# Kernel tuning notes

Hardware: AMD Instinct MI355X
Metric: run time of the kernel (lower is better)

The kernel has to match this reference:

```python
import jax, jax.numpy as jnp
import numpy as np

B, S, Dm, H, W, G = 2, 4096, 768, 12, 256, 16
HD = Dm // H
NEG = -10000.0


def _band_qk(q, k, w):
    # q,k: [B,S,H,D] -> banded scores [B,S,H,2w+1]; slot j = key position i-w+j
    Bq, Sq, Hq, Dq = q.shape
    nb = Sq // w
    qb = q.reshape(Bq, nb, w, Hq, Dq)
    kp = jnp.pad(k, ((0, 0), (w, w), (0, 0), (0, 0)))
    idx = (jnp.arange(nb) * w)[:, None] + jnp.arange(3 * w)[None, :]
    kb = kp[:, idx]                                    # [B,nb,3w,H,D]
    s = jnp.einsum('btxhd,btyhd->bthxy', qb, kb)       # [B,nb,H,w,3w]
    r = jnp.arange(w)[:, None]
    c = r + jnp.arange(2 * w + 1)[None, :]
    band = s[..., r, c]                                # [B,nb,H,w,2w+1]
    return band.transpose(0, 1, 3, 2, 4).reshape(Bq, Sq, Hq, 2 * w + 1)


def _band_pv(p, v, w):
    # p: [B,S,H,2w+1], v: [B,S,H,D] -> [B,S,H,D]
    Bp, Sp, Hp, _ = p.shape
    Dv = v.shape[-1]
    nb = Sp // w
    vp = jnp.pad(v, ((0, 0), (w, w), (0, 0), (0, 0)))
    idx = (jnp.arange(nb) * w)[:, None] + jnp.arange(3 * w)[None, :]
    vb = vp[:, idx]                                    # [B,nb,3w,H,D]
    pb = p.reshape(Bp, nb, w, Hp, 2 * w + 1).transpose(0, 1, 3, 2, 4)
    r = jnp.arange(w)[:, None]
    c = r + jnp.arange(2 * w + 1)[None, :]
    pband = jnp.zeros((Bp, nb, Hp, w, 3 * w), p.dtype).at[..., r, c].set(pb)
    out = jnp.einsum('bthxy,btyhd->btxhd', pband, vb)  # [B,nb,w,H,D]
    return out.reshape(Bp, Sp, Hp, Dv)


def setup_inputs() -> dict:
    key = jax.random.key(0)
    ks = jax.random.split(key, 13)
    inp = {'hidden_states': jax.random.normal(ks[0], (B, S, Dm), dtype=jnp.float32)}
    names = ['Wq', 'bq', 'Wk', 'bk', 'Wv', 'bv', 'Wqg', 'bqg', 'Wkg', 'bkg', 'Wvg', 'bvg']
    for i, n in enumerate(names):
        sh = (Dm, Dm) if n.startswith('W') else (Dm,)
        inp[n] = 0.02 * jax.random.normal(ks[i + 1], sh, dtype=jnp.float32)
    inp['n_global'] = G
    return inp


def reference(hidden_states, Wq, bq, Wk, bk, Wv, bv, Wqg, bqg, Wkg, bkg, Wvg, bvg, n_global):
    Bh, Sh, D = hidden_states.shape
    hd = D // H
    w, g = W, n_global
    scale = 1.0 / jnp.sqrt(jnp.float32(hd))
    q = ((hidden_states @ Wq + bq) * scale).reshape(Bh, Sh, H, hd)
    k = (hidden_states @ Wk + bk).reshape(Bh, Sh, H, hd)
    v = (hidden_states @ Wv + bv).reshape(Bh, Sh, H, hd)
    # banded local attention scores (mask_invalid_locations -> -inf outside seq)
    band = _band_qk(q, k, w)                           # [B,S,H,2w+1]
    i = jnp.arange(Sh)[:, None]
    j = jnp.arange(2 * w + 1)[None, :]
    kpos = i - w + j                                   # key position per window slot
    valid = (kpos >= 0) & (kpos < Sh)
    band = jnp.where(valid[None, :, None, :], band, -jnp.inf)
    # remove global keys from windowed attention (-10000 float mask)
    band = band + jnp.where(valid & (kpos < g), NEG, 0.0)[None, :, None, :]
    # global columns: every query attends to global keys (local k projection)
    sel = jnp.einsum('bihd,bghd->bihg', q, k[:, :g])
    logits = jnp.concatenate([sel, band], axis=-1)     # [B,S,H,g+2w+1]
    probs = jax.nn.softmax(logits.astype(jnp.float32), axis=-1)
    attn = jnp.einsum('bihg,bghd->bihd', probs[..., :g], v[:, :g])
    attn = attn + _band_pv(probs[..., g:], v, w)       # [B,S,H,hd]
    # global token rows: full attention with global projections
    qg = ((hidden_states[:, :g] @ Wqg + bqg) * scale).reshape(Bh, g, H, hd)
    kg = (hidden_states @ Wkg + bkg).reshape(Bh, Sh, H, hd)
    vg = (hidden_states @ Wvg + bvg).reshape(Bh, Sh, H, hd)
    gl = jnp.einsum('bghd,bshd->bhgs', qg, kg)
    gp = jax.nn.softmax(gl.astype(jnp.float32), axis=-1)
    out_g = jnp.einsum('bhgs,bshd->bghd', gp, vg)      # [B,g,H,hd]
    attn = attn.at[:, :g].set(out_g)
    return attn.reshape(Bh, Sh, D)
```

## Files before the change

### kernel.cpp

```cpp
#include <hip/hip_runtime.h>

constexpr int Bc = 2, Sc = 4096, Dmc = 768, Hc = 12, HDc = 64, Wc = 256, Gc = 16;
constexpr int NCH = 16, CHK = 256;
constexpr float LOG2E = 1.4426950408889634f;
constexpr float SCALEc = 0.125f;
constexpr float SCALE2q = 0.125f * LOG2E;
constexpr float NEG2c = -10000.0f * LOG2E;

typedef __attribute__((ext_vector_type(8))) short s16x8;
typedef __attribute__((ext_vector_type(4))) short s16x4;
typedef __attribute__((ext_vector_type(4))) float f32x4;
typedef __attribute__((ext_vector_type(2))) unsigned int u32x2;

#define DEVINL __device__ __forceinline__

DEVINL float b2f(short x) {
  unsigned int u = ((unsigned int)(unsigned short)x) << 16;
  return __builtin_bit_cast(float, u);
}
DEVINL short f2b(float f) {
  unsigned int u = __builtin_bit_cast(unsigned int, f);
  unsigned int r = (u + 0x7fffu + ((u >> 16) & 1u)) >> 16;
  return (short)r;
}
DEVINL void gload16(const short* g, const short* l) {
  __builtin_amdgcn_global_load_lds(
      (const __attribute__((address_space(1))) void*)g,
      (__attribute__((address_space(3))) void*)l, 16, 0, 0);
}

__global__ __launch_bounds__(256) void conv_bf16(
    const float* __restrict__ src, short* __restrict__ dst)
{
  const size_t i = ((size_t)blockIdx.x * 256 + threadIdx.x) * 8;
  f32x4 a = *(const f32x4*)(src + i);
  f32x4 c = *(const f32x4*)(src + i + 4);
  s16x8 r;
#pragma unroll
  for (int u = 0; u < 4; ++u) { r[u] = f2b(a[u]); r[4 + u] = f2b(c[u]); }
  *(s16x8*)(dst + i) = r;
}

__global__ __launch_bounds__(256) void transpose_w(
    const float* __restrict__ W0, const float* __restrict__ W1, const float* __restrict__ W2,
    short* __restrict__ T0, short* __restrict__ T1, short* __restrict__ T2)
{
  const float* W = blockIdx.z == 0 ? W0 : (blockIdx.z == 1 ? W1 : W2);
  short* T = blockIdx.z == 0 ? T0 : (blockIdx.z == 1 ? T1 : T2);
  __shared__ short t[32][33];
  const int k0 = blockIdx.x * 32, n0 = blockIdx.y * 32;
  const int a = threadIdx.x >> 3, cg = (threadIdx.x & 7) * 4;
  f32x4 v = *(const f32x4*)&W[(size_t)(k0 + a) * Dmc + n0 + cg];
#pragma unroll
  for (int u = 0; u < 4; ++u) t[a][cg + u] = f2b(v[u]);
  __syncthreads();
  s16x4 s;
#pragma unroll
  for (int u = 0; u < 4; ++u) s[u] = t[cg + u][a];
  *(s16x4*)&T[(size_t)(n0 + a) * Dmc + k0 + cg] = s;
}

__global__ __launch_bounds__(256) void gemm_fused(
    const short* __restrict__ X, const short* __restrict__ Wt,
    const float* __restrict__ b0, const float* __restrict__ b1, const float* __restrict__ b2,
    short* __restrict__ Y0, float scale0)
{
  __shared__ short lds[24576];
  char* ldsb = (char*)lds;
  const int tid = threadIdx.x, lane = tid & 63, wid = tid >> 6;
  const int gy = gridDim.y;

  const int rawd = blockIdx.x + 64 * blockIdx.y;
  const int wgid = (rawd & 7) * (gy * 8) + (rawd >> 3);
  const int mi0 = wgid / gy, ny = wgid - mi0 * gy;
  const int m0 = mi0 * 128;
  const int nch = ny / 12, ncol = (ny % 12) * 64;
  const int n0g = ny * 64;

  short* Y = Y0 + (size_t)nch * 6291456;
  const float* bias = nch == 0 ? b0 : (nch == 1 ? b1 : b2);
  const float scale = nch == 0 ? scale0 : 1.0f;

  const int lr = lane & 15, lq = lane >> 4;
  const int wm = (wid & 1) * 64, wn = (wid >> 1) * 32;

  const int l8 = lane >> 3, l7 = lane & 7;
  const int colsh = ((l7 * 16) ^ (l8 << 4)) >> 1;
  const short* Aptr[4];
  const short* Bptr[2];
#pragma unroll
  for (int i = 0; i < 4; ++i)
    Aptr[i] = X + (size_t)(m0 + wid * 32 + i * 8 + l8) * Dmc + colsh;
#pragma unroll
  for (int i = 0; i < 2; ++i)
    Bptr[i] = Wt + (size_t)(n0g + wid * 16 + i * 8 + l8) * Dmc + colsh;

  int arb[4][2], brb[2][2];
#pragma unroll
  for (int mi = 0; mi < 4; ++mi)
#pragma unroll
    for (int ks = 0; ks < 2; ++ks) {
      int row = wm + mi * 16 + lr;
      arb[mi][ks] = row * 128 + ((lq * 16 + ks * 64) ^ ((row & 7) << 4));
    }
#pragma unroll
  for (int ni = 0; ni < 2; ++ni)
#pragma unroll
    for (int ks = 0; ks < 2; ++ks) {
      int row = wn + ni * 16 + lr;
      brb[ni][ks] = 16384 + row * 128 + ((lq * 16 + ks * 64) ^ ((row & 7) << 4));
    }

  f32x4 acc[4][2] = {};

  auto issue = [&](int kt, int buf) {
    const int ko = kt * 64, bo = buf * 12288;
#pragma unroll
    for (int i = 0; i < 4; ++i) gload16(Aptr[i] + ko, &lds[bo + wid * 2048 + i * 512]);
#pragma unroll
    for (int i = 0; i < 2; ++i) gload16(Bptr[i] + ko, &lds[bo + 8192 + wid * 1024 + i * 512]);
  };

  issue(0, 0);
  for (int kt = 0; kt < 12; ++kt) {
    const int buf = kt & 1, bo = buf * 24576;
    asm volatile("s_waitcnt vmcnt(0)" ::: "memory");
    __syncthreads();
    if (kt < 11) issue(kt + 1, buf ^ 1);
#pragma unroll
    for (int ks = 0; ks < 2; ++ks) {
      s16x8 af[4], bf[2];
#pragma unroll
      for (int mi = 0; mi < 4; ++mi) af[mi] = *(const s16x8*)(ldsb + bo + arb[mi][ks]);
#pragma unroll
      for (int ni = 0; ni < 2; ++ni) bf[ni] = *(const s16x8*)(ldsb + bo + brb[ni][ks]);
#pragma unroll
      for (int mi = 0; mi < 4; ++mi)
#pragma unroll
        for (int ni = 0; ni < 2; ++ni)
          acc[mi][ni] = __builtin_amdgcn_mfma_f32_16x16x32_bf16(af[mi], bf[ni], acc[mi][ni], 0, 0, 0);
    }
  }

#pragma unroll
  for (int mi = 0; mi < 4; ++mi)
#pragma unroll
    for (int ni = 0; ni < 2; ++ni) {
      int col = ncol + wn + ni * 16 + lr;
      float bv_ = bias[col];
#pragma unroll
      for (int r = 0; r < 4; ++r) {
        int row = m0 + wm + mi * 16 + lq * 4 + r;
        Y[(size_t)row * Dmc + col] = f2b((acc[mi][ni][r] + bv_) * scale);
      }
    }
}

__global__ __launch_bounds__(256) void qg_proj(
    const float* __restrict__ hs, const float* __restrict__ Wqg,
    const float* __restrict__ bqg, float* __restrict__ qg)
{
  const int row = blockIdx.x;
  const int b = row / Gc, i = row % Gc;
  const int tid = threadIdx.x;
  const int n = blockIdx.y * 128 + (tid & 127);
  const int half = tid >> 7;
  __shared__ float x[Dmc];
  __shared__ float part[128];
  for (int c = tid; c < Dmc; c += 256)
    x[c] = b2f(f2b(hs[((size_t)(b * Sc + i)) * Dmc + c]));
  __syncthreads();
  float acc = 0.f;
#pragma unroll 4
  for (int c = half * 384; c < half * 384 + 384; ++c)
    acc = fmaf(x[c], b2f(f2b(Wqg[(size_t)c * Dmc + n])), acc);
  if (half) part[tid & 127] = acc;
  __syncthreads();
  if (!half)
    qg[(size_t)row * Dmc + n] = (acc + part[tid] + bqg[n]) * SCALE2q;
}

__global__ __launch_bounds__(256) void local_attn_mfma(
    const short* __restrict__ q, const short* __restrict__ k,
    const short* __restrict__ v, float* __restrict__ out)
{
  const int raw = blockIdx.x + 64 * (blockIdx.y + 12 * blockIdx.z);
  const int swz = (raw & 7) * 192 + (raw >> 3);
  const int q0 = (swz & 63) * 64;
  const int h = (swz >> 6) % 12, b = swz / 768;
  const int tid = threadIdx.x, lane = tid & 63, wid = tid >> 6;

  __shared__ short Ks[4096];
  __shared__ short Vt[4096];
  __shared__ short Ps[4][1024];
  char* KsB = (char*)Ks;
  char* VtB = (char*)Vt;

  const int ql = lane & 15;
  const int lg = lane >> 4;
  const int qr = wid * 16 + ql;

  s16x8 qf[2];
  {
    const short* qp = q + ((size_t)(b * Sc + q0 + qr)) * Dmc + h * HDc + lg * 8;
    qf[0] = *(const s16x8*)qp;
    qf[1] = *(const s16x8*)(qp + 32);
  }

  f32x4 oacc[4] = {};
  float m_run = -INFINITY, l_run = 0.f;

  const int krow = tid >> 3, kcol16 = (tid & 7) * 16;
  const int vp = tid & 31, vo = tid >> 5;
  const size_t hoff = (size_t)h * HDc;
  const size_t brow = (size_t)b * Sc;

  auto keyof = [&](int c) {
    int key = (c < Gc) ? c : q0 - 272 + c;
    return min(max(key, 0), Sc - 1);
  };

  s16x8 kreg0, kreg1, vreg0, vreg1;
  auto loadRegs = [&](int ch) {
    kreg0 = *(const s16x8*)(k + (brow + keyof(ch * 64 + krow))      * Dmc + hoff + (kcol16 >> 1));
    kreg1 = *(const s16x8*)(k + (brow + keyof(ch * 64 + 32 + krow)) * Dmc + hoff + (kcol16 >> 1));
    vreg0 = *(const s16x8*)(v + (brow + keyof(ch * 64 + 2 * vp))     * Dmc + hoff + vo * 8);
    vreg1 = *(const s16x8*)(v + (brow + keyof(ch * 64 + 2 * vp + 1)) * Dmc + hoff + vo * 8);
  };

  loadRegs(0);

  for (int ch = 0; ch < 10; ++ch) {
    __syncthreads();
    *(s16x8*)(KsB + krow * 128        + (kcol16 ^ ((krow & 7) << 4))) = kreg0;
    *(s16x8*)(KsB + (krow + 32) * 128 + (kcol16 ^ ((krow & 7) << 4))) = kreg1;
#pragma unroll
    for (int j = 0; j < 8; ++j) {
      int d = vo * 8 + j;
      unsigned int wrd = (unsigned int)(unsigned short)vreg0[j] |
                         ((unsigned int)(unsigned short)vreg1[j] << 16);
      *(unsigned int*)(VtB + d * 128 + ((4 * vp) ^ (j << 4))) = wrd;
    }
    if (ch < 9) loadRegs(ch + 1);
    __syncthreads();

    f32x4 sac[4] = {};
#pragma unroll
    for (int kt = 0; kt < 4; ++kt) {
      int row = kt * 16 + ql;
#pragma unroll
      for (int sl = 0; sl < 2; ++sl) {
        s16x8 af = *(const s16x8*)(KsB + row * 128 + ((lg * 16 + sl * 64) ^ ((row & 7) << 4)));
        sac[kt] = __builtin_amdgcn_mfma_f32_16x16x32_bf16(af, qf[sl], sac[kt], 0, 0, 0);
      }
    }

    bool needMask = (ch < 2) | (ch > 7) | (q0 < 272) | (q0 > Sc - 384);
    if (needMask) {
#pragma unroll
      for (int kt = 0; kt < 4; ++kt)
#pragma unroll
        for (int r = 0; r < 4; ++r) {
          int c = ch * 64 + kt * 16 + lg * 4 + r;
          if (c >= Gc) {
            float sv = sac[kt][r];
            int jj = c - Gc - qr;
            int kp2 = q0 - 272 + c;
            bool ok = (jj >= 0) & (jj <= 2 * Wc) & (kp2 >= 0) & (kp2 < Sc);
            sac[kt][r] = ok ? (sv + ((kp2 < Gc) ? NEG2c : 0.f)) : -INFINITY;
          }
        }
    }

    float cm = -INFINITY;
#pragma unroll
    for (int kt = 0; kt < 4; ++kt)
#pragma unroll
      for (int r = 0; r < 4; ++r) cm = fmaxf(cm, sac[kt][r]);
    cm = fmaxf(cm, __shfl_xor(cm, 16));
    cm = fmaxf(cm, __shfl_xor(cm, 32));

    if (__all(cm <= m_run + 11.5f)) {
      float cl = 0.f;
#pragma unroll
      for (int kt = 0; kt < 4; ++kt)
#pragma unroll
        for (int r = 0; r < 4; ++r) {
          float p = exp2f(sac[kt][r] - m_run);
          sac[kt][r] = p;
          cl += p;
        }
      cl += __shfl_xor(cl, 16);
      cl += __shfl_xor(cl, 32);
      l_run += cl;
    } else {
      float m_new = fmaxf(m_run, cm);
      float scale = exp2f(m_run - m_new);
      float cl = 0.f;
#pragma unroll
      for (int kt = 0; kt < 4; ++kt)
#pragma unroll
        for (int r = 0; r < 4; ++r) {
          float p = exp2f(sac[kt][r] - m_new);
          sac[kt][r] = p;
          cl += p;
        }
      cl += __shfl_xor(cl, 16);
      cl += __shfl_xor(cl, 32);
      l_run = l_run * scale + cl;
      m_run = m_new;
#pragma unroll
      for (int rr = 0; rr < 4; ++rr) {
        float os = __shfl(scale, lg * 4 + rr);
#pragma unroll
        for (int dt = 0; dt < 4; ++dt) oacc[dt][rr] *= os;
      }
    }

    char* PsB = (char*)Ps[wid];
#pragma unroll
    for (int kt = 0; kt < 4; ++kt) {
      u32x2 pw;
      asm("v_cvt_pk_bf16_f32 %0, %1, %2" : "=v"(pw.x) : "v"(sac[kt][0]), "v"(sac[kt][1]));
      asm("v_cvt_pk_bf16_f32 %0, %1, %2" : "=v"(pw.y) : "v"(sac[kt][2]), "v"(sac[kt][3]));
      *(u32x2*)(PsB + ql * 128 + ((kt * 32 + lg * 8) ^ ((ql & 7) << 4))) = pw;
    }
    s16x8 pf[2];
#pragma unroll
    for (int ks = 0; ks < 2; ++ks)
      pf[ks] = *(const s16x8*)(PsB + ql * 128 + ((ks * 64 + lg * 16) ^ ((ql & 7) << 4)));
#pragma unroll
    for (int dt = 0; dt < 4; ++dt) {
      int d = dt * 16 + ql;
#pragma unroll
      for (int ks = 0; ks < 2; ++ks) {
        s16x8 vf = *(const s16x8*)(VtB + d * 128 + ((ks * 64 + lg * 16) ^ ((d & 7) << 4)));
        oacc[dt] = __builtin_amdgcn_mfma_f32_16x16x32_bf16(pf[ks], vf, oacc[dt], 0, 0, 0);
      }
    }
  }

  float inv = 1.f / l_run;
#pragma unroll
  for (int rr = 0; rr < 4; ++rr) {
    float oi = __shfl(inv, lg * 4 + rr);
    int row = q0 + wid * 16 + lg * 4 + rr;
    float* op = out + ((size_t)(b * Sc + row)) * Dmc + h * HDc + ql;
#pragma unroll
    for (int dt = 0; dt < 4; ++dt)
      op[dt * 16] = oacc[dt][rr] * oi;
  }
}

__global__ __launch_bounds__(256) void global_attn_part(
    const float* __restrict__ qg, const short* __restrict__ kg,
    const short* __restrict__ vg, float* __restrict__ pml, float* __restrict__ po)
{
  const int ch = blockIdx.x & (NCH - 1);
  const int i  = blockIdx.x >> 4;
  const int h = blockIdx.y, b = blockIdx.z;
  const int tid = threadIdx.x, lane = tid & 63, wid = tid >> 6;

  __shared__ float qrow[64];
  __shared__ float pls[CHK];
  __shared__ float red[8];
  __shared__ float osum[4][64];

  if (tid < 64) qrow[tid] = qg[(size_t)(b * Gc + i) * Dmc + h * HDc + tid];
  __syncthreads();

  const int sk = ch * CHK + tid;
  const s16x8* kr = (const s16x8*)(kg + ((size_t)(b * Sc + sk)) * Dmc + h * HDc);
  float acc = 0.f;
#pragma unroll
  for (int c = 0; c < 8; ++c) {
    s16x8 kv = kr[c];
#pragma unroll
    for (int u = 0; u < 8; ++u) acc = fmaf(qrow[c * 8 + u], b2f(kv[u]), acc);
  }

  float m = acc;
#pragma unroll
  for (int off = 32; off > 0; off >>= 1) m = fmaxf(m, __shfl_xor(m, off));
  if (lane == 0) red[wid] = m;
  __syncthreads();
  m = fmaxf(fmaxf(red[0], red[1]), fmaxf(red[2], red[3]));

  float p = exp2f(acc - m);
  pls[tid] = p;
  float ls = p;
#pragma unroll
  for (int off = 32; off > 0; off >>= 1) ls += __shfl_xor(ls, off);
  if (lane == 0) red[4 + wid] = ls;
  __syncthreads();
  const float l = red[4] + red[5] + red[6] + red[7];

  const int jg = tid >> 3, db = (tid & 7) * 8;
  float o[8] = {};
  const short* vb2 = vg + ((size_t)(b * Sc + ch * CHK + jg * 8)) * Dmc + h * HDc + db;
#pragma unroll
  for (int jj = 0; jj < 8; ++jj) {
    float pw = pls[jg * 8 + jj];
    s16x8 vv = *(const s16x8*)(vb2 + (size_t)jj * Dmc);
#pragma unroll
    for (int u = 0; u < 8; ++u) o[u] = fmaf(pw, b2f(vv[u]), o[u]);
  }
#pragma unroll
  for (int mk = 8; mk <= 32; mk <<= 1)
#pragma unroll
    for (int u = 0; u < 8; ++u) o[u] += __shfl_xor(o[u], mk);
  if ((lane & 56) == 0) {
#pragma unroll
    for (int u = 0; u < 8; ++u) osum[wid][(lane & 7) * 8 + u] = o[u];
  }
  __syncthreads();

  const size_t slot = (((size_t)(b * Hc + h) * Gc + i) * NCH + ch);
  if (tid < 64)
    po[slot * 64 + tid] = osum[0][tid] + osum[1][tid] + osum[2][tid] + osum[3][tid];
  if (tid == 0) { pml[slot * 2] = m; pml[slot * 2 + 1] = l; }
}

__global__ __launch_bounds__(64) void global_attn_comb(
    const float* __restrict__ pml, const float* __restrict__ po,
    float* __restrict__ out)
{
  const int i = blockIdx.x, h = blockIdx.y, b = blockIdx.z;
  const int d = threadIdx.x;
  const size_t base = ((size_t)(b * Hc + h) * Gc + i) * NCH;

  float m = -INFINITY;
#pragma unroll
  for (int ch = 0; ch < NCH; ++ch) m = fmaxf(m, pml[(base + ch) * 2]);
  float l = 0.f, o = 0.f;
#pragma unroll
  for (int ch = 0; ch < NCH; ++ch) {
    float wgt = exp2f(pml[(base + ch) * 2] - m);
    l = fmaf(pml[(base + ch) * 2 + 1], wgt, l);
    o = fmaf(po[(base + ch) * 64 + d], wgt, o);
  }
  out[((size_t)(b * Sc + i)) * Dmc + h * HDc + d] = o / l;
}

extern "C" void kernel_launch(void* const* d_in, const int* in_sizes, int n_in,
                              void* d_out, int out_size, void* d_ws, size_t ws_size,
                              hipStream_t stream) {
  const float* hs  = (const float*)d_in[0];
  const float* Wq  = (const float*)d_in[1];
  const float* bq  = (const float*)d_in[2];
  const float* Wk  = (const float*)d_in[3];
  const float* bk  = (const float*)d_in[4];
  const float* Wv  = (const float*)d_in[5];
  const float* bv  = (const float*)d_in[6];
  const float* Wqg = (const float*)d_in[7];
  const float* bqg = (const float*)d_in[8];
  const float* Wkg = (const float*)d_in[9];
  const float* bkg = (const float*)d_in[10];
  const float* Wvg = (const float*)d_in[11];
  const float* bvg = (const float*)d_in[12];
  float* out = (float*)d_out;

  char* ws = (char*)d_ws;
  const size_t bufB = (size_t)Bc * Sc * Dmc * sizeof(short);
  short* hsb = (short*)(ws);
  short* s1  = (short*)(ws + bufB);
  short* s2  = (short*)(ws + 2 * bufB);
  short* s3  = (short*)(ws + 3 * bufB);

  short* wtA = (short*)d_out;
  short* wtB = wtA + (size_t)Dmc * Dmc;
  short* wtC = wtB + (size_t)Dmc * Dmc;
  float* qg  = (float*)(ws + 3 * bufB);
  float* pml = (float*)(ws + 3 * bufB + 98304);
  float* po  = (float*)(ws + 3 * bufB + 147456);
  short* wtD = (short*)(ws + 3 * bufB + (4u << 20));
  short* wtE = wtD + (size_t)Dmc * Dmc;

  dim3 bb(256);
  conv_bf16<<<dim3(3072), bb, 0, stream>>>(hs, hsb);
  transpose_w<<<dim3(24, 24, 3), bb, 0, stream>>>(Wq, Wk, Wv, wtA, wtB, wtC);

  gemm_fused<<<dim3(64, 36), bb, 0, stream>>>(hsb, wtA, bq, bk, bv, s1, SCALE2q);

  local_attn_mfma<<<dim3(64, Hc, Bc), bb, 0, stream>>>(s1, s2, s3, out);

  transpose_w<<<dim3(24, 24, 2), bb, 0, stream>>>(Wkg, Wvg, Wvg, wtD, wtE, wtE);
  gemm_fused<<<dim3(64, 24), bb, 0, stream>>>(hsb, wtD, bkg, bvg, bvg, s1, 1.0f);

  qg_proj<<<dim3(Bc * Gc, Dmc / 128), bb, 0, stream>>>(hs, Wqg, bqg, qg);
  global_attn_part<<<dim3(Gc * NCH, Hc, Bc), bb, 0, stream>>>(qg, s1, s2, pml, po);
  global_attn_comb<<<dim3(Gc, Hc, Bc), dim3(64), 0, stream>>>(pml, po, out);
}
```

Before: 200.2 us.

## Process 128 queries per block so each wave reuses K/V tiles twice

```diff
diff --git a/kernel.cpp b/kernel.cpp
--- a/kernel.cpp
+++ b/kernel.cpp
@@ -3,7 +3,6 @@
 constexpr int Bc = 2, Sc = 4096, Dmc = 768, Hc = 12, HDc = 64, Wc = 256, Gc = 16;
 constexpr int NCH = 16, CHK = 256;
 constexpr float LOG2E = 1.4426950408889634f;
-constexpr float SCALEc = 0.125f;
 constexpr float SCALE2q = 0.125f * LOG2E;
 constexpr float NEG2c = -10000.0f * LOG2E;
 
@@ -184,31 +183,31 @@
     const short* __restrict__ q, const short* __restrict__ k,
     const short* __restrict__ v, float* __restrict__ out)
 {
-  const int raw = blockIdx.x + 64 * (blockIdx.y + 12 * blockIdx.z);
-  const int swz = (raw & 7) * 192 + (raw >> 3);
-  const int q0 = (swz & 63) * 64;
-  const int h = (swz >> 6) % 12, b = swz / 768;
+  const int raw = blockIdx.x + 32 * (blockIdx.y + 12 * blockIdx.z);
+  const int swz = (raw & 7) * 96 + (raw >> 3);
+  const int q0 = (swz & 31) * 128;
+  const int h = (swz >> 5) % 12, b = swz / 384;
   const int tid = threadIdx.x, lane = tid & 63, wid = tid >> 6;
 
   __shared__ short Ks[4096];
   __shared__ short Vt[4096];
-  __shared__ short Ps[4][1024];
+  __shared__ short Ps[4][2048];
   char* KsB = (char*)Ks;
   char* VtB = (char*)Vt;
 
   const int ql = lane & 15;
   const int lg = lane >> 4;
-  const int qr = wid * 16 + ql;
-
-  s16x8 qf[2];
-  {
-    const short* qp = q + ((size_t)(b * Sc + q0 + qr)) * Dmc + h * HDc + lg * 8;
-    qf[0] = *(const s16x8*)qp;
-    qf[1] = *(const s16x8*)(qp + 32);
-  }
-
-  f32x4 oacc[4] = {};
-  float m_run = -INFINITY, l_run = 0.f;
+
+  s16x8 qf[2][2];
+#pragma unroll
+  for (int t = 0; t < 2; ++t) {
+    const short* qp = q + ((size_t)(b * Sc + q0 + wid * 32 + t * 16 + ql)) * Dmc + h * HDc + lg * 8;
+    qf[t][0] = *(const s16x8*)qp;
+    qf[t][1] = *(const s16x8*)(qp + 32);
+  }
+
+  f32x4 oacc[2][4] = {};
+  float m_run[2] = {-INFINITY, -INFINITY}, l_run[2] = {0.f, 0.f};
 
   const int krow = tid >> 3, kcol16 = (tid & 7) * 16;
   const int vp = tid & 31, vo = tid >> 5;
@@ -230,7 +229,7 @@
 
   loadRegs(0);
 
-  for (int ch = 0; ch < 10; ++ch) {
+  for (int ch = 0; ch < 11; ++ch) {
     __syncthreads();
     *(s16x8*)(KsB + krow * 128        + (kcol16 ^ ((krow & 7) << 4))) = kreg0;
     *(s16x8*)(KsB + (krow + 32) * 128 + (kcol16 ^ ((krow & 7) << 4))) = kreg1;
@@ -241,114 +240,138 @@
                          ((unsigned int)(unsigned short)vreg1[j] << 16);
       *(unsigned int*)(VtB + d * 128 + ((4 * vp) ^ (j << 4))) = wrd;
     }
-    if (ch < 9) loadRegs(ch + 1);
+    if (ch < 10) loadRegs(ch + 1);
     __syncthreads();
 
-    f32x4 sac[4] = {};
+    f32x4 sac[2][4] = {};
 #pragma unroll
     for (int kt = 0; kt < 4; ++kt) {
       int row = kt * 16 + ql;
 #pragma unroll
       for (int sl = 0; sl < 2; ++sl) {
         s16x8 af = *(const s16x8*)(KsB + row * 128 + ((lg * 16 + sl * 64) ^ ((row & 7) << 4)));
-        sac[kt] = __builtin_amdgcn_mfma_f32_16x16x32_bf16(af, qf[sl], sac[kt], 0, 0, 0);
-      }
-    }
-
-    bool needMask = (ch < 2) | (ch > 7) | (q0 < 272) | (q0 > Sc - 384);
+        sac[0][kt] = __builtin_amdgcn_mfma_f32_16x16x32_bf16(af, qf[0][sl], sac[0][kt], 0, 0, 0);
+        sac[1][kt] = __builtin_amdgcn_mfma_f32_16x16x32_bf16(af, qf[1][sl], sac[1][kt], 0, 0, 0);
+      }
+    }
+
+    bool needMask = (ch < 3) | (ch > 7) | (q0 < 272) | (q0 > Sc - 433);
     if (needMask) {
 #pragma unroll
+      for (int t = 0; t < 2; ++t) {
+        int qr = wid * 32 + t * 16 + ql;
+#pragma unroll
+        for (int kt = 0; kt < 4; ++kt)
+#pragma unroll
+          for (int r = 0; r < 4; ++r) {
+            int c = ch * 64 + kt * 16 + lg * 4 + r;
+            if (c >= Gc) {
+              float sv = sac[t][kt][r];
+              int jj = c - Gc - qr;
+              int kp2 = q0 - 272 + c;
+              bool ok = (jj >= 0) & (jj <= 2 * Wc) & (kp2 >= 0) & (kp2 < Sc);
+              sac[t][kt][r] = ok ? (sv + ((kp2 < Gc) ? NEG2c : 0.f)) : -INFINITY;
+            }
+          }
+      }
+    }
+
+    float cm[2];
+#pragma unroll
+    for (int t = 0; t < 2; ++t) {
+      float m_ = -INFINITY;
+#pragma unroll
       for (int kt = 0; kt < 4; ++kt)
 #pragma unroll
-        for (int r = 0; r < 4; ++r) {
-          int c = ch * 64 + kt * 16 + lg * 4 + r;
-          if (c >= Gc) {
-            float sv = sac[kt][r];
-            int jj = c - Gc - qr;
-            int kp2 = q0 - 272 + c;
-            bool ok = (jj >= 0) & (jj <= 2 * Wc) & (kp2 >= 0) & (kp2 < Sc);
-            sac[kt][r] = ok ? (sv + ((kp2 < Gc) ? NEG2c : 0.f)) : -INFINITY;
+        for (int r = 0; r < 4; ++r) m_ = fmaxf(m_, sac[t][kt][r]);
+      m_ = fmaxf(m_, __shfl_xor(m_, 16));
+      m_ = fmaxf(m_, __shfl_xor(m_, 32));
+      cm[t] = m_;
+    }
+
+    if (__all((cm[0] <= m_run[0] + 11.5f) & (cm[1] <= m_run[1] + 11.5f))) {
+#pragma unroll
+      for (int t = 0; t < 2; ++t) {
+        float cl = 0.f;
+#pragma unroll
+        for (int kt = 0; kt < 4; ++kt)
+#pragma unroll
+          for (int r = 0; r < 4; ++r) {
+            float p = exp2f(sac[t][kt][r] - m_run[t]);
+            sac[t][kt][r] = p;
+            cl += p;
           }
+        cl += __shfl_xor(cl, 16);
+        cl += __shfl_xor(cl, 32);
+        l_run[t] += cl;
+      }
+    } else {
+#pragma unroll
+      for (int t = 0; t < 2; ++t) {
+        float m_new = fmaxf(m_run[t], cm[t]);
+        float scale = exp2f(m_run[t] - m_new);
+        float cl = 0.f;
+#pragma unroll
+        for (int kt = 0; kt < 4; ++kt)
+#pragma unroll
+          for (int r = 0; r < 4; ++r) {
+            float p = exp2f(sac[t][kt][r] - m_new);
+            sac[t][kt][r] = p;
+            cl += p;
+          }
+        cl += __shfl_xor(cl, 16);
+        cl += __shfl_xor(cl, 32);
+        l_run[t] = l_run[t] * scale + cl;
+        m_run[t] = m_new;
+#pragma unroll
+        for (int rr = 0; rr < 4; ++rr) {
+          float os = __shfl(scale, lg * 4 + rr);
+#pragma unroll
+          for (int dt = 0; dt < 4; ++dt) oacc[t][dt][rr] *= os;
         }
-    }
-
-    float cm = -INFINITY;
-#pragma unroll
-    for (int kt = 0; kt < 4; ++kt)
-#pragma unroll
-      for (int r = 0; r < 4; ++r) cm = fmaxf(cm, sac[kt][r]);
-    cm = fmaxf(cm, __shfl_xor(cm, 16));
-    cm = fmaxf(cm, __shfl_xor(cm, 32));
-
-    if (__all(cm <= m_run + 11.5f)) {
-      float cl = 0.f;
-#pragma unroll
-      for (int kt = 0; kt < 4; ++kt)
-#pragma unroll
-        for (int r = 0; r < 4; ++r) {
-          float p = exp2f(sac[kt][r] - m_run);
-          sac[kt][r] = p;
-          cl += p;
-        }
-      cl += __shfl_xor(cl, 16);
-      cl += __shfl_xor(cl, 32);
-      l_run += cl;
-    } else {
-      float m_new = fmaxf(m_run, cm);
-      float scale = exp2f(m_run - m_new);
-      float cl = 0.f;
-#pragma unroll
-      for (int kt = 0; kt < 4; ++kt)
-#pragma unroll
-        for (int r = 0; r < 4; ++r) {
-          float p = exp2f(sac[kt][r] - m_new);
-          sac[kt][r] = p;
-          cl += p;
-        }
-      cl += __shfl_xor(cl, 16);
-      cl += __shfl_xor(cl, 32);
-      l_run = l_run * scale + cl;
-      m_run = m_new;
-#pragma unroll
-      for (int rr = 0; rr < 4; ++rr) {
-        float os = __shfl(scale, lg * 4 + rr);
-#pragma unroll
-        for (int dt = 0; dt < 4; ++dt) oacc[dt][rr] *= os;
       }
     }
 
     char* PsB = (char*)Ps[wid];
 #pragma unroll
-    for (int kt = 0; kt < 4; ++kt) {
-      u32x2 pw;
-      asm("v_cvt_pk_bf16_f32 %0, %1, %2" : "=v"(pw.x) : "v"(sac[kt][0]), "v"(sac[kt][1]));
-      asm("v_cvt_pk_bf16_f32 %0, %1, %2" : "=v"(pw.y) : "v"(sac[kt][2]), "v"(sac[kt][3]));
-      *(u32x2*)(PsB + ql * 128 + ((kt * 32 + lg * 8) ^ ((ql & 7) << 4))) = pw;
-    }
-    s16x8 pf[2];
-#pragma unroll
-    for (int ks = 0; ks < 2; ++ks)
-      pf[ks] = *(const s16x8*)(PsB + ql * 128 + ((ks * 64 + lg * 16) ^ ((ql & 7) << 4)));
+    for (int t = 0; t < 2; ++t)
+#pragma unroll
+      for (int kt = 0; kt < 4; ++kt) {
+        u32x2 pw;
+        asm("v_cvt_pk_bf16_f32 %0, %1, %2" : "=v"(pw.x) : "v"(sac[t][kt][0]), "v"(sac[t][kt][1]));
+        asm("v_cvt_pk_bf16_f32 %0, %1, %2" : "=v"(pw.y) : "v"(sac[t][kt][2]), "v"(sac[t][kt][3]));
+        *(u32x2*)(PsB + t * 2048 + ql * 128 + ((kt * 32 + lg * 8) ^ ((ql & 7) << 4))) = pw;
+      }
+    s16x8 pf[2][2];
+#pragma unroll
+    for (int t = 0; t < 2; ++t)
+#pragma unroll
+      for (int ks = 0; ks < 2; ++ks)
+        pf[t][ks] = *(const s16x8*)(PsB + t * 2048 + ql * 128 + ((ks * 64 + lg * 16) ^ ((ql & 7) << 4)));
 #pragma unroll
     for (int dt = 0; dt < 4; ++dt) {
       int d = dt * 16 + ql;
 #pragma unroll
       for (int ks = 0; ks < 2; ++ks) {
         s16x8 vf = *(const s16x8*)(VtB + d * 128 + ((ks * 64 + lg * 16) ^ ((d & 7) << 4)));
-        oacc[dt] = __builtin_amdgcn_mfma_f32_16x16x32_bf16(pf[ks], vf, oacc[dt], 0, 0, 0);
-      }
-    }
-  }
-
-  float inv = 1.f / l_run;
-#pragma unroll
-  for (int rr = 0; rr < 4; ++rr) {
-    float oi = __shfl(inv, lg * 4 + rr);
-    int row = q0 + wid * 16 + lg * 4 + rr;
-    float* op = out + ((size_t)(b * Sc + row)) * Dmc + h * HDc + ql;
-#pragma unroll
-    for (int dt = 0; dt < 4; ++dt)
-      op[dt * 16] = oacc[dt][rr] * oi;
+        oacc[0][dt] = __builtin_amdgcn_mfma_f32_16x16x32_bf16(pf[0][ks], vf, oacc[0][dt], 0, 0, 0);
+        oacc[1][dt] = __builtin_amdgcn_mfma_f32_16x16x32_bf16(pf[1][ks], vf, oacc[1][dt], 0, 0, 0);
+      }
+    }
+  }
+
+#pragma unroll
+  for (int t = 0; t < 2; ++t) {
+    float inv = 1.f / l_run[t];
+#pragma unroll
+    for (int rr = 0; rr < 4; ++rr) {
+      float oi = __shfl(inv, lg * 4 + rr);
+      int row = q0 + wid * 32 + t * 16 + lg * 4 + rr;
+      float* op = out + ((size_t)(b * Sc + row)) * Dmc + h * HDc + ql;
+#pragma unroll
+      for (int dt = 0; dt < 4; ++dt)
+        op[dt * 16] = oacc[t][dt][rr] * oi;
+    }
   }
 }
 
@@ -482,7 +505,7 @@
 
   gemm_fused<<<dim3(64, 36), bb, 0, stream>>>(hsb, wtA, bq, bk, bv, s1, SCALE2q);
 
-  local_attn_mfma<<<dim3(64, Hc, Bc), bb, 0, stream>>>(s1, s2, s3, out);
+  local_attn_mfma<<<dim3(32, Hc, Bc), bb, 0, stream>>>(s1, s2, s3, out);
 
   transpose_w<<<dim3(24, 24, 2), bb, 0, stream>>>(Wkg, Wvg, Wvg, wtD, wtE, wtE);
   gemm_fused<<<dim3(64, 24), bb, 0, stream>>>(hsb, wtD, bkg, bvg, bvg, s1, 1.0f);
```

Measured after the change: 208.1 us. 3.9% more time.
